# Optimization experiments

Measured on AMD Instinct MI355X. Metric: run time of the kernel, lower is better.

The kernel has to match this reference:

```python
import jax, jax.numpy as jnp
import numpy as np
from jax.experimental.jet import jet

ORDER = 3  # Taylor order from init_kwargs
D, C, H = 4096, 4096, 8192


def setup_inputs() -> dict:
    key = jax.random.key(0)
    k = jax.random.split(key, 6)
    sc1 = 1.0 / np.sqrt(D + C)
    sc2 = 1.0 / np.sqrt(H)
    return {
        "h": jax.random.normal(k[0], (D,), jnp.float32),
        "r": jnp.zeros((), jnp.float32),  # ignored residual slot of h_r tuple
        "t": jax.random.uniform(k[1], (), jnp.float32),
        "c": jax.random.normal(k[2], (C,), jnp.float32),
        "W1": jax.random.normal(k[3], (D + C, H), jnp.float32) * sc1,
        "b1": jnp.zeros((H,), jnp.float32),
        "W2": jax.random.normal(k[4], (H, D), jnp.float32) * sc2,
        "b2": jnp.zeros((D,), jnp.float32),
    }


def reference(h, r, t, c, W1, b1, W2, b2):
    # dynamics f(h, t, c): 2-layer tanh MLP on concat(h, c)
    def f(_h, _t, _c):
        x = jnp.concatenate((_h, _c))
        return jnp.tanh(x @ W1 + b1) @ W2 + b2

    h_shape = h.shape

    def g(h_t):
        # expand flattened state+time through dynamics
        _h, _t = jnp.reshape(h_t[:-1], h_shape), h_t[-1]
        dh = jnp.ravel(f(_h, _t, c))
        return jnp.concatenate((dh, jnp.array([1.0], dtype=dh.dtype)))

    h_t = jnp.concatenate((jnp.ravel(h), jnp.reshape(t, (1,))))
    # recursive Taylor-mode jet expansion
    (y0, [*yns]) = jet(g, (h_t,), ((jnp.ones_like(h_t),),))
    for _ in range(ORDER - 1):
        (y0, [*yns]) = jet(g, (h_t,), ((y0, *yns),))
    dydt = jnp.reshape(y0[:-1], h_shape)
    drdt = jnp.reshape(yns[-2][:-1], h_shape)
    return (dydt, jnp.mean(drdt ** 2))
```

## Files before the change

kernel.cpp:

```cpp
#include <hip/hip_runtime.h>

#define DD 4096
#define HH 8192
#define NSPLIT 128

enum Stage { S_X0 = 0, S_TANH, S_BIASOUT, S_PMUL, S_COPY, S_S2 };

__device__ inline unsigned short f2bf(float f) {
    unsigned int u = __float_as_uint(f);
    u += 0x7FFFu + ((u >> 16) & 1u);
    return (unsigned short)(u >> 16);
}

template <int STAGE, int KS, int SPREV, int KPREV, int NTOT, int CPT>
__global__ __launch_bounds__(256) void gemv_f32(
    const float* __restrict__ W, const float* __restrict__ Pprev,
    float* __restrict__ Pout, unsigned short* __restrict__ Wb, int convRows,
    const float* __restrict__ h, const float* __restrict__ c,
    const float* __restrict__ b1,
    float* __restrict__ s0g, float* __restrict__ t0g)
{
    constexpr int GROUPS = 256 / KS;
    __shared__ float xs[KS];
    __shared__ float part[GROUPS][KS];
    const int tid = threadIdx.x;
    const int k0 = blockIdx.y * KS;

    if constexpr (STAGE == S_X0) {
        if (tid < KS) {
            int k = k0 + tid;
            xs[tid] = (k < DD) ? h[k] : c[k - DD];
        }
    } else {
        const int g = tid / KS;
        const int j = tid % KS;
        float acc = 0.f;
        for (int s = g; s < SPREV; s += GROUPS)
            acc += Pprev[(size_t)s * KPREV + k0 + j];
        part[g][j] = acc;
        __syncthreads();
        if (tid < KS) {
            const int k = k0 + tid;
            float tot = 0.f;
#pragma unroll
            for (int g2 = 0; g2 < GROUPS; ++g2) tot += part[g2][tid];
            float s = tanhf(tot + b1[k]);
            xs[tid] = s;
            if (blockIdx.x == 0) { s0g[k] = s; t0g[k] = 1.f - s * s; }
        }
    }
    __syncthreads();

    const bool doConv = (k0 < convRows);

    if constexpr (CPT == 4) {
        const int ncol = blockIdx.x * 1024 + tid * 4;
        const float* Wp = W + (size_t)k0 * NTOT + ncol;
        float ax = 0.f, ay = 0.f, az = 0.f, aw = 0.f;
#pragma unroll 4
        for (int k = 0; k < KS; ++k) {
            float xv = xs[k];
            float4 w = *reinterpret_cast<const float4*>(Wp + (size_t)k * NTOT);
            ax = fmaf(xv, w.x, ax);
            ay = fmaf(xv, w.y, ay);
            az = fmaf(xv, w.z, az);
            aw = fmaf(xv, w.w, aw);
            if (doConv) {
                ushort4 o;
                o.x = f2bf(w.x); o.y = f2bf(w.y); o.z = f2bf(w.z); o.w = f2bf(w.w);
                *reinterpret_cast<ushort4*>(Wb + (size_t)(k0 + k) * NTOT + ncol) = o;
            }
        }
        *reinterpret_cast<float4*>(Pout + (size_t)blockIdx.y * NTOT + ncol) =
            make_float4(ax, ay, az, aw);
    } else {
        const int ncol = blockIdx.x * 512 + tid * 2;
        const float* Wp = W + (size_t)k0 * NTOT + ncol;
        float ax = 0.f, ay = 0.f;
#pragma unroll 4
        for (int k = 0; k < KS; ++k) {
            float xv = xs[k];
            float2 w = *reinterpret_cast<const float2*>(Wp + (size_t)k * NTOT);
            ax = fmaf(xv, w.x, ax);
            ay = fmaf(xv, w.y, ay);
            if (doConv) {
                ushort2 o;
                o.x = f2bf(w.x); o.y = f2bf(w.y);
                *reinterpret_cast<ushort2*>(Wb + (size_t)(k0 + k) * NTOT + ncol) = o;
            }
        }
        *reinterpret_cast<float2*>(Pout + (size_t)blockIdx.y * NTOT + ncol) =
            make_float2(ax, ay);
    }
}

template <int STAGE, int KS, int SPREV, int KPREV, int NTOT>
__global__ __launch_bounds__(256) void gemv_b16(
    const unsigned short* __restrict__ Wb, const float* __restrict__ Pprev,
    float* __restrict__ Pout,
    const float* __restrict__ b2, const float* __restrict__ s0g,
    const float* __restrict__ t0g, float* __restrict__ a1g,
    float* __restrict__ outv)
{
    constexpr int GROUPS = 256 / KS;
    __shared__ float xs[KS];
    __shared__ float part[GROUPS][KS];
    const int tid = threadIdx.x;
    const int k0 = blockIdx.y * KS;

    {
        const int g = tid / KS;
        const int j = tid % KS;
        float acc = 0.f;
        for (int s = g; s < SPREV; s += GROUPS)
            acc += Pprev[(size_t)s * KPREV + k0 + j];
        part[g][j] = acc;
        __syncthreads();
        if (tid < KS) {
            const int k = k0 + tid;
            float tot = 0.f;
#pragma unroll
            for (int g2 = 0; g2 < GROUPS; ++g2) tot += part[g2][tid];
            float xv;
            if constexpr (STAGE == S_BIASOUT) {
                xv = tot + b2[k];
                if (blockIdx.x == 0) outv[k] = xv;
            } else if constexpr (STAGE == S_PMUL) {
                xv = t0g[k] * tot;
                if (blockIdx.x == 0) a1g[k] = tot;
            } else if constexpr (STAGE == S_COPY) {
                xv = tot;
            } else {
                float a1v = a1g[k];
                xv = t0g[k] * (tot - s0g[k] * a1v * a1v);
            }
            xs[tid] = xv;
        }
    }
    __syncthreads();

    const int ncol = blockIdx.x * 1024 + tid * 4;
    const unsigned short* Wp = Wb + (size_t)k0 * NTOT + ncol;
    float ax = 0.f, ay = 0.f, az = 0.f, aw = 0.f;
#pragma unroll 8
    for (int k = 0; k < KS; ++k) {
        float xv = xs[k];
        uint2 w = *reinterpret_cast<const uint2*>(Wp + (size_t)k * NTOT);
        float w0 = __uint_as_float(w.x << 16);
        float w1 = __uint_as_float(w.x & 0xFFFF0000u);
        float w2 = __uint_as_float(w.y << 16);
        float w3 = __uint_as_float(w.y & 0xFFFF0000u);
        ax = fmaf(xv, w0, ax);
        ay = fmaf(xv, w1, ay);
        az = fmaf(xv, w2, az);
        aw = fmaf(xv, w3, aw);
    }
    *reinterpret_cast<float4*>(Pout + (size_t)blockIdx.y * NTOT + ncol) =
        make_float4(ax, ay, az, aw);
}

__global__ __launch_bounds__(256) void reduce_C2(const float* __restrict__ P6,
                                                 float* __restrict__ C2) {
    int n = blockIdx.x * 256 + threadIdx.x;
    float acc = 0.f;
#pragma unroll 8
    for (int s = 0; s < NSPLIT; ++s) acc += P6[(size_t)s * DD + n];
    C2[n] = acc;
}

__global__ __launch_bounds__(256) void reduce_meansq(const float* __restrict__ C2v,
                                                     float* __restrict__ dout) {
    float s = 0.f;
    for (int i = threadIdx.x; i < DD; i += 256) {
        float v = C2v[i];
        s = fmaf(v, v, s);
    }
    for (int off = 32; off; off >>= 1) s += __shfl_down(s, off);
    __shared__ float ls[4];
    int wid = threadIdx.x >> 6;
    if ((threadIdx.x & 63) == 0) ls[wid] = s;
    __syncthreads();
    if (threadIdx.x == 0) dout[DD] = (ls[0] + ls[1] + ls[2] + ls[3]) / (float)DD;
}

extern "C" void kernel_launch(void* const* d_in, const int* in_sizes, int n_in,
                              void* d_out, int out_size, void* d_ws, size_t ws_size,
                              hipStream_t stream) {
    const float* h  = (const float*)d_in[0];
    const float* c  = (const float*)d_in[3];
    const float* W1 = (const float*)d_in[4];
    const float* b1 = (const float*)d_in[5];
    const float* W2 = (const float*)d_in[6];
    const float* b2 = (const float*)d_in[7];
    float* out = (float*)d_out;
    float* ws = (float*)d_ws;

    float* P1 = ws;
    float* P2 = P1 + 1048576;
    float* P3 = P2 + 524288;
    float* P4 = P3 + 1048576;
    float* P5 = P4 + 524288;
    float* P6 = P5 + 1048576;
    float* s0 = P6 + 524288;
    float* t0 = s0 + 8192;
    float* a1 = t0 + 8192;
    float* C2 = a1 + 8192;
    unsigned short* W1b = (unsigned short*)(C2 + 4096);
    unsigned short* W2b = W1b + (size_t)DD * HH;

    gemv_f32<S_X0, 64, 1, 1, HH, 4><<<dim3(8, NSPLIT), 256, 0, stream>>>(
        W1, nullptr, P1, W1b, DD, h, c, b1, s0, t0);
    gemv_f32<S_TANH, 64, NSPLIT, HH, DD, 2><<<dim3(8, NSPLIT), 256, 0, stream>>>(
        W2, P1, P2, W2b, HH, h, c, b1, s0, t0);
    gemv_b16<S_BIASOUT, 32, NSPLIT, DD, HH><<<dim3(8, NSPLIT), 256, 0, stream>>>(
        W1b, P2, P3, b2, s0, t0, a1, out);
    gemv_b16<S_PMUL, 64, NSPLIT, HH, DD><<<dim3(4, NSPLIT), 256, 0, stream>>>(
        W2b, P3, P4, b2, s0, t0, a1, out);
    gemv_b16<S_COPY, 32, NSPLIT, DD, HH><<<dim3(8, NSPLIT), 256, 0, stream>>>(
        W1b, P4, P5, b2, s0, t0, a1, out);
    gemv_b16<S_S2, 64, NSPLIT, HH, DD><<<dim3(4, NSPLIT), 256, 0, stream>>>(
        W2b, P5, P6, b2, s0, t0, a1, out);
    reduce_C2<<<16, 256, 0, stream>>>(P6, C2);
    reduce_meansq<<<1, 256, 0, stream>>>(C2, out);
}
```

Measured before the change: 237.9 us.

## Widen bf16 GEMV loads, retile split-K grids, use nontemporal fp32 weight loads

The bf16 GEMV kernels now load 8 bf16 weights per thread with 16-byte loads and keep 8 accumulators, and each block covers 2048 columns. The split-K factors and grid shapes of all stages are retiled so more, smaller K slices run in parallel, and the partial-sum buffers grow to match. The fp32 conversion pass drops its 2-column path in favour of one 4-column path that uses nontemporal loads. The aim is more bytes in flight per thread and better occupancy in these memory-bound GEMVs, at the cost of larger partial-sum buffers and more reduction work in the next stage.

```diff
diff --git a/kernel.cpp b/kernel.cpp
--- a/kernel.cpp
+++ b/kernel.cpp
@@ -2,9 +2,10 @@
 
 #define DD 4096
 #define HH 8192
-#define NSPLIT 128
 
 enum Stage { S_X0 = 0, S_TANH, S_BIASOUT, S_PMUL, S_COPY, S_S2 };
+
+typedef float vfloat4 __attribute__((ext_vector_type(4)));
 
 __device__ inline unsigned short f2bf(float f) {
     unsigned int u = __float_as_uint(f);
@@ -12,7 +13,11 @@
     return (unsigned short)(u >> 16);
 }
 
-template <int STAGE, int KS, int SPREV, int KPREV, int NTOT, int CPT>
+__device__ inline vfloat4 ldnt4(const float* p) {
+    return __builtin_nontemporal_load(reinterpret_cast<const vfloat4*>(p));
+}
+
+template <int STAGE, int KS, int SPREV, int KPREV, int NTOT>
 __global__ __launch_bounds__(256) void gemv_f32(
     const float* __restrict__ W, const float* __restrict__ Pprev,
     float* __restrict__ Pout, unsigned short* __restrict__ Wb, int convRows,
@@ -52,46 +57,25 @@
     __syncthreads();
 
     const bool doConv = (k0 < convRows);
-
-    if constexpr (CPT == 4) {
-        const int ncol = blockIdx.x * 1024 + tid * 4;
-        const float* Wp = W + (size_t)k0 * NTOT + ncol;
-        float ax = 0.f, ay = 0.f, az = 0.f, aw = 0.f;
+    const int ncol = blockIdx.x * 1024 + tid * 4;
+    const float* Wp = W + (size_t)k0 * NTOT + ncol;
+    float ax = 0.f, ay = 0.f, az = 0.f, aw = 0.f;
 #pragma unroll 4
-        for (int k = 0; k < KS; ++k) {
-            float xv = xs[k];
-            float4 w = *reinterpret_cast<const float4*>(Wp + (size_t)k * NTOT);
-            ax = fmaf(xv, w.x, ax);
-            ay = fmaf(xv, w.y, ay);
-            az = fmaf(xv, w.z, az);
-            aw = fmaf(xv, w.w, aw);
-            if (doConv) {
-                ushort4 o;
-                o.x = f2bf(w.x); o.y = f2bf(w.y); o.z = f2bf(w.z); o.w = f2bf(w.w);
-                *reinterpret_cast<ushort4*>(Wb + (size_t)(k0 + k) * NTOT + ncol) = o;
-            }
-        }
-        *reinterpret_cast<float4*>(Pout + (size_t)blockIdx.y * NTOT + ncol) =
-            make_float4(ax, ay, az, aw);
-    } else {
-        const int ncol = blockIdx.x * 512 + tid * 2;
-        const float* Wp = W + (size_t)k0 * NTOT + ncol;
-        float ax = 0.f, ay = 0.f;
-#pragma unroll 4
-        for (int k = 0; k < KS; ++k) {
-            float xv = xs[k];
-            float2 w = *reinterpret_cast<const float2*>(Wp + (size_t)k * NTOT);
-            ax = fmaf(xv, w.x, ax);
-            ay = fmaf(xv, w.y, ay);
-            if (doConv) {
-                ushort2 o;
-                o.x = f2bf(w.x); o.y = f2bf(w.y);
-                *reinterpret_cast<ushort2*>(Wb + (size_t)(k0 + k) * NTOT + ncol) = o;
-            }
-        }
-        *reinterpret_cast<float2*>(Pout + (size_t)blockIdx.y * NTOT + ncol) =
-            make_float2(ax, ay);
-    }
+    for (int k = 0; k < KS; ++k) {
+        float xv = xs[k];
+        vfloat4 w = ldnt4(Wp + (size_t)k * NTOT);
+        ax = fmaf(xv, w.x, ax);
+        ay = fmaf(xv, w.y, ay);
+        az = fmaf(xv, w.z, az);
+        aw = fmaf(xv, w.w, aw);
+        if (doConv) {
+            ushort4 o;
+            o.x = f2bf(w.x); o.y = f2bf(w.y); o.z = f2bf(w.z); o.w = f2bf(w.w);
+            *reinterpret_cast<ushort4*>(Wb + (size_t)(k0 + k) * NTOT + ncol) = o;
+        }
+    }
+    *reinterpret_cast<float4*>(Pout + (size_t)blockIdx.y * NTOT + ncol) =
+        make_float4(ax, ay, az, aw);
 }
 
 template <int STAGE, int KS, int SPREV, int KPREV, int NTOT>
@@ -139,32 +123,35 @@
     }
     __syncthreads();
 
-    const int ncol = blockIdx.x * 1024 + tid * 4;
+    const int ncol = blockIdx.x * 2048 + tid * 8;
     const unsigned short* Wp = Wb + (size_t)k0 * NTOT + ncol;
-    float ax = 0.f, ay = 0.f, az = 0.f, aw = 0.f;
-#pragma unroll 8
+    float a0 = 0.f, a1 = 0.f, a2 = 0.f, a3 = 0.f;
+    float a4 = 0.f, a5 = 0.f, a6 = 0.f, a7 = 0.f;
+#pragma unroll 4
     for (int k = 0; k < KS; ++k) {
         float xv = xs[k];
-        uint2 w = *reinterpret_cast<const uint2*>(Wp + (size_t)k * NTOT);
-        float w0 = __uint_as_float(w.x << 16);
-        float w1 = __uint_as_float(w.x & 0xFFFF0000u);
-        float w2 = __uint_as_float(w.y << 16);
-        float w3 = __uint_as_float(w.y & 0xFFFF0000u);
-        ax = fmaf(xv, w0, ax);
-        ay = fmaf(xv, w1, ay);
-        az = fmaf(xv, w2, az);
-        aw = fmaf(xv, w3, aw);
-    }
-    *reinterpret_cast<float4*>(Pout + (size_t)blockIdx.y * NTOT + ncol) =
-        make_float4(ax, ay, az, aw);
-}
-
+        uint4 w = *reinterpret_cast<const uint4*>(Wp + (size_t)k * NTOT);
+        a0 = fmaf(xv, __uint_as_float(w.x << 16), a0);
+        a1 = fmaf(xv, __uint_as_float(w.x & 0xFFFF0000u), a1);
+        a2 = fmaf(xv, __uint_as_float(w.y << 16), a2);
+        a3 = fmaf(xv, __uint_as_float(w.y & 0xFFFF0000u), a3);
+        a4 = fmaf(xv, __uint_as_float(w.z << 16), a4);
+        a5 = fmaf(xv, __uint_as_float(w.z & 0xFFFF0000u), a5);
+        a6 = fmaf(xv, __uint_as_float(w.w << 16), a6);
+        a7 = fmaf(xv, __uint_as_float(w.w & 0xFFFF0000u), a7);
+    }
+    float* op = Pout + (size_t)blockIdx.y * NTOT + ncol;
+    *reinterpret_cast<float4*>(op)     = make_float4(a0, a1, a2, a3);
+    *reinterpret_cast<float4*>(op + 4) = make_float4(a4, a5, a6, a7);
+}
+
+template <int SPREV>
 __global__ __launch_bounds__(256) void reduce_C2(const float* __restrict__ P6,
                                                  float* __restrict__ C2) {
     int n = blockIdx.x * 256 + threadIdx.x;
     float acc = 0.f;
 #pragma unroll 8
-    for (int s = 0; s < NSPLIT; ++s) acc += P6[(size_t)s * DD + n];
+    for (int s = 0; s < SPREV; ++s) acc += P6[(size_t)s * DD + n];
     C2[n] = acc;
 }
 
@@ -197,29 +184,29 @@
 
     float* P1 = ws;
     float* P2 = P1 + 1048576;
-    float* P3 = P2 + 524288;
-    float* P4 = P3 + 1048576;
-    float* P5 = P4 + 524288;
-    float* P6 = P5 + 1048576;
-    float* s0 = P6 + 524288;
+    float* P3 = P2 + 1048576;
+    float* P4 = P3 + 2097152;
+    float* P5 = P4 + 2097152;
+    float* P6 = P5 + 2097152;
+    float* s0 = P6 + 2097152;
     float* t0 = s0 + 8192;
     float* a1 = t0 + 8192;
     float* C2 = a1 + 8192;
     unsigned short* W1b = (unsigned short*)(C2 + 4096);
     unsigned short* W2b = W1b + (size_t)DD * HH;
 
-    gemv_f32<S_X0, 64, 1, 1, HH, 4><<<dim3(8, NSPLIT), 256, 0, stream>>>(
+    gemv_f32<S_X0, 64, 1, 1, HH><<<dim3(8, 128), 256, 0, stream>>>(
         W1, nullptr, P1, W1b, DD, h, c, b1, s0, t0);
-    gemv_f32<S_TANH, 64, NSPLIT, HH, DD, 2><<<dim3(8, NSPLIT), 256, 0, stream>>>(
+    gemv_f32<S_TANH, 32, 128, HH, DD><<<dim3(4, 256), 256, 0, stream>>>(
         W2, P1, P2, W2b, HH, h, c, b1, s0, t0);
-    gemv_b16<S_BIASOUT, 32, NSPLIT, DD, HH><<<dim3(8, NSPLIT), 256, 0, stream>>>(
+    gemv_b16<S_BIASOUT, 16, 256, DD, HH><<<dim3(4, 256), 256, 0, stream>>>(
         W1b, P2, P3, b2, s0, t0, a1, out);
-    gemv_b16<S_PMUL, 64, NSPLIT, HH, DD><<<dim3(4, NSPLIT), 256, 0, stream>>>(
+    gemv_b16<S_PMUL, 16, 256, HH, DD><<<dim3(2, 512), 256, 0, stream>>>(
         W2b, P3, P4, b2, s0, t0, a1, out);
-    gemv_b16<S_COPY, 32, NSPLIT, DD, HH><<<dim3(8, NSPLIT), 256, 0, stream>>>(
+    gemv_b16<S_COPY, 16, 512, DD, HH><<<dim3(4, 256), 256, 0, stream>>>(
         W1b, P4, P5, b2, s0, t0, a1, out);
-    gemv_b16<S_S2, 64, NSPLIT, HH, DD><<<dim3(4, NSPLIT), 256, 0, stream>>>(
+    gemv_b16<S_S2, 16, 256, HH, DD><<<dim3(2, 512), 256, 0, stream>>>(
         W2b, P5, P6, b2, s0, t0, a1, out);
-    reduce_C2<<<16, 256, 0, stream>>>(P6, C2);
+    reduce_C2<512><<<16, 256, 0, stream>>>(P6, C2);
     reduce_meansq<<<1, 256, 0, stream>>>(C2, out);
 }
```

New measurement: 223.4 us. 6.1% less time.
